# Kernel tuning notes

Hardware: AMD Instinct MI355X
Metric: run time of the kernel (lower is better)

The kernel has to match this reference:

```python
import jax, jax.numpy as jnp
import numpy as np

D = 1024
H = 16
DK = D // H

def setup_inputs() -> dict:
    key = jax.random.key(0)
    k1, k2, k3 = jax.random.split(key, 3)
    x = jax.random.normal(k1, (2, 2048, D), dtype=jnp.float32)
    # torch nn.Linear weight shapes: qkv [3D, D], o [D, D]; y = x @ W.T
    scale = 1.0 / np.sqrt(D)
    W_qkv = jax.random.normal(k2, (3 * D, D), dtype=jnp.float32) * scale
    W_o = jax.random.normal(k3, (D, D), dtype=jnp.float32) * scale
    return {"x": x, "W_qkv": W_qkv, "W_o": W_o}

def reference(x, W_qkv, W_o):
    B, T, _ = x.shape
    qkv = x @ W_qkv.T                                    # [B, T, 3D]
    qkv = qkv.reshape(B, T, 3, H, DK)
    qkv = jnp.transpose(qkv, (0, 3, 2, 1, 4))            # [B, H, 3, T, DK]
    q, k, v = qkv[:, :, 0], qkv[:, :, 1], qkv[:, :, 2]   # each [B, H, T, DK]
    scores = jnp.einsum("bhqd,bhkd->bhqk", q, k) / np.sqrt(DK)
    causal = jnp.tril(jnp.ones((T, T), dtype=bool))       # keep lower triangle
    scores = jnp.where(causal, scores, -jnp.inf)
    attn = jax.nn.softmax(scores, axis=-1)
    out = jnp.einsum("bhqk,bhkd->bhqd", attn, v)          # [B, H, T, DK]
    out = jnp.transpose(out, (0, 2, 1, 3)).reshape(B, T, H * DK)
    return out @ W_o.T
```

## Files before the change

### kernel.cpp

```cpp
#include <hip/hip_runtime.h>
#include <hip/hip_bf16.h>

typedef __bf16 bf16x8 __attribute__((ext_vector_type(8)));
typedef float f32x4 __attribute__((ext_vector_type(4)));
typedef unsigned int u32;
typedef u32 u32x4 __attribute__((ext_vector_type(4)));

#define MFMA(a, b, c) __builtin_amdgcn_mfma_f32_16x16x32_bf16((a), (b), (c), 0, 0, 0)

static __device__ __forceinline__ bf16x8 ld8(const __bf16* p) {
  return *reinterpret_cast<const bf16x8*>(p);
}

static __device__ __forceinline__ u32 pkbf(float a, float b) {
  union { __bf16 h; unsigned short s; } x, y;
  x.h = (__bf16)a; y.h = (__bf16)b;
  return (u32)x.s | ((u32)y.s << 16);
}

typedef unsigned int __attribute__((address_space(1))) gu32_t;
typedef unsigned int __attribute__((address_space(3))) lu32_t;
static __device__ __forceinline__ void gld16(const __bf16* g, __bf16* l) {
  __builtin_amdgcn_global_load_lds((const gu32_t*)(const void*)g,
                                   (lu32_t*)(void*)l, 16, 0, 0);
}

__global__ __launch_bounds__(256)
void cvt_f32_bf16(const float* __restrict__ a, __bf16* __restrict__ oa, int na,
                  const float* __restrict__ b, __bf16* __restrict__ ob) {
  const int i = blockIdx.x * 256 + threadIdx.x;
  const float* src; __bf16* dst; int e;
  if (i < (na >> 3)) { src = a; dst = oa; e = i << 3; }
  else { src = b; dst = ob; e = (i << 3) - na; }
  f32x4 v0 = *reinterpret_cast<const f32x4*>(src + e);
  f32x4 v1 = *reinterpret_cast<const f32x4*>(src + e + 4);
  bf16x8 o;
#pragma unroll
  for (int j = 0; j < 4; ++j) { o[j] = (__bf16)v0[j]; o[j + 4] = (__bf16)v1[j]; }
  *reinterpret_cast<bf16x8*>(dst + e) = o;
}

static __device__ __forceinline__ void stage8f(__bf16* __restrict__ dst,
                                               const float* __restrict__ src) {
  f32x4 a = *reinterpret_cast<const f32x4*>(src);
  f32x4 b = *reinterpret_cast<const f32x4*>(src + 4);
  bf16x8 o;
#pragma unroll
  for (int i = 0; i < 4; ++i) { o[i] = (__bf16)a[i]; o[i + 4] = (__bf16)b[i]; }
  *reinterpret_cast<bf16x8*>(dst) = o;
}

template<int BN, bool SPLIT, bool OUT_BF16, bool B_F32>
__global__ __launch_bounds__(256, 2)
void gemm3(const __bf16* __restrict__ A, const void* __restrict__ Wv,
           void* __restrict__ Cv, __bf16* __restrict__ VT,
           int M, int N, int K) {
  constexpr int NF = BN / 32;
  constexpr float SC2Q = 0.125f * 1.4426950408889634f;
  __shared__ __bf16 lA[128 * 64];
  __shared__ __bf16 lB[BN * 64];

  const int tid = threadIdx.x;
  const int ntiles = N / BN;
  const int mt = blockIdx.x / ntiles;
  const int nt = blockIdx.x % ntiles;
  const int m0 = mt << 7, n0 = nt * BN;
  const int lane = tid & 63, w = tid >> 6;
  const int wm = (w >> 1) << 6;
  const int wn = (w & 1) * (BN / 2);
  const int fr = lane & 15, fg = lane >> 4;

  f32x4 acc[4][NF] = {};

  for (int k0 = 0; k0 < K; k0 += 64) {
    __syncthreads();
#pragma unroll
    for (int jj = 0; jj < 4; ++jj) {
      const int q = (w << 2) | jj;
      const int v = (q << 6) | lane;
      const int row = v >> 3;
      const int cc = (v & 7) ^ (row & 7);
      gld16(A + (size_t)(m0 + row) * K + k0 + (cc << 3), lA + (q << 9));
    }
    if constexpr (B_F32) {
#pragma unroll
      for (int hh = 0; hh < BN / 64; ++hh) {
        const int row = (tid >> 2) + (hh << 6);
        const int c0 = (tid & 3) << 1;
        const float* src = (const float*)Wv + (size_t)(n0 + row) * K + k0 + (c0 << 3);
#pragma unroll
        for (int cg = 0; cg < 2; ++cg)
          stage8f(lB + (row << 6) + (((c0 + cg) ^ (row & 7)) << 3), src + (cg << 3));
      }
    } else {
#pragma unroll
      for (int jj = 0; jj < NF; ++jj) {
        const int q = w * NF + jj;
        const int v = (q << 6) | lane;
        const int row = v >> 3;
        const int cc = (v & 7) ^ (row & 7);
        gld16((const __bf16*)Wv + (size_t)(n0 + row) * K + k0 + (cc << 3), lB + (q << 9));
      }
    }
    __syncthreads();

    bf16x8 af[2][4], bfr[2][NF];
#pragma unroll
    for (int kc = 0; kc < 2; ++kc) {
#pragma unroll
      for (int m = 0; m < 4; ++m) {
        const int row = wm + m * 16 + fr;
        af[kc][m] = ld8(lA + (row << 6) + ((((kc << 2) | fg) ^ (row & 7)) << 3));
      }
#pragma unroll
      for (int n = 0; n < NF; ++n) {
        const int row = wn + n * 16 + fr;
        bfr[kc][n] = ld8(lB + (row << 6) + ((((kc << 2) | fg) ^ (row & 7)) << 3));
      }
    }
#pragma unroll
    for (int kc = 0; kc < 2; ++kc)
#pragma unroll
      for (int m = 0; m < 4; ++m)
#pragma unroll
        for (int n = 0; n < NF; ++n)
          acc[m][n] = MFMA(af[kc][m], bfr[kc][n], acc[m][n]);
  }

#pragma unroll
  for (int m = 0; m < 4; ++m) {
#pragma unroll
    for (int n = 0; n < NF; ++n) {
#pragma unroll
      for (int r = 0; r < 4; ++r) {
        int row = m0 + wm + m * 16 + fg * 4 + r;
        int col = n0 + wn + n * 16 + fr;
        float v = acc[m][n][r];
        if constexpr (SPLIT) {
          int b = row >> 11, t = row & 2047;
          if (col >= 2048) {
            VT[((size_t)(b << 10) + (col - 2048)) * 2048 + t] = (__bf16)v;
          } else {
            if (col < 1024) v *= SC2Q;
            ((__bf16*)Cv)[(size_t)row * 2048 + col] = (__bf16)v;
          }
        } else if constexpr (OUT_BF16) {
          ((__bf16*)Cv)[(size_t)row * N + col] = (__bf16)v;
        } else {
          ((float*)Cv)[(size_t)row * N + col] = v;
        }
      }
    }
  }
}

static __device__ __forceinline__ void softmax_step(
    f32x4 (&s)[4], f32x4 (&o)[4], float& m, float& l, bf16x8 (&pa)[2],
    bool diag, int q0wt, int k0, int fg, int fr) {
  constexpr float NEG = -1e30f;
  float sv[4][4];
#pragma unroll
  for (int n = 0; n < 4; ++n)
#pragma unroll
    for (int r = 0; r < 4; ++r) {
      float x = s[n][r];
      if (diag && (k0 + n * 16 + fg * 4 + r > q0wt + fr)) x = NEG;
      sv[n][r] = x;
    }

  float t0 = fmaxf(fmaxf(sv[0][0], sv[0][1]), fmaxf(sv[0][2], sv[0][3]));
  float t1 = fmaxf(fmaxf(sv[1][0], sv[1][1]), fmaxf(sv[1][2], sv[1][3]));
  float t2 = fmaxf(fmaxf(sv[2][0], sv[2][1]), fmaxf(sv[2][2], sv[2][3]));
  float t3 = fmaxf(fmaxf(sv[3][0], sv[3][1]), fmaxf(sv[3][2], sv[3][3]));
  float rm = fmaxf(fmaxf(t0, t1), fmaxf(t2, t3));
  rm = fmaxf(rm, __shfl_xor(rm, 16));
  rm = fmaxf(rm, __shfl_xor(rm, 32));

  if (!__all(rm <= m + 16.f)) {
    float mnew = fmaxf(m, rm);
    float alpha = __builtin_exp2f(m - mnew);
    m = mnew;
    l *= alpha;
    float ao[4];
#pragma unroll
    for (int r = 0; r < 4; ++r)
      ao[r] = __shfl(alpha, fg * 4 + r);
#pragma unroll
    for (int n = 0; n < 4; ++n)
#pragma unroll
      for (int r = 0; r < 4; ++r)
        o[n][r] *= ao[r];
  }

  float p[4][4];
#pragma unroll
  for (int n = 0; n < 4; ++n)
#pragma unroll
    for (int r = 0; r < 4; ++r)
      p[n][r] = __builtin_exp2f(sv[n][r] - m);

  float u0 = (p[0][0] + p[0][1]) + (p[0][2] + p[0][3]);
  float u1 = (p[1][0] + p[1][1]) + (p[1][2] + p[1][3]);
  float u2 = (p[2][0] + p[2][1]) + (p[2][2] + p[2][3]);
  float u3 = (p[3][0] + p[3][1]) + (p[3][2] + p[3][3]);
  float rs = (u0 + u1) + (u2 + u3);
  rs += __shfl_xor(rs, 16);
  rs += __shfl_xor(rs, 32);
  l += rs;

  u32 wpk[4][2];
#pragma unroll
  for (int n = 0; n < 4; ++n) {
    wpk[n][0] = pkbf(p[n][0], p[n][1]);
    wpk[n][1] = pkbf(p[n][2], p[n][3]);
  }

  u32 rcv[2][2][2];
#pragma unroll
  for (int e = 0; e < 2; ++e) {
    const int src = fr + ((((fg & 1) << 1) | ((fg >> 1) ^ e)) << 4);
    const bool tsel = ((fg & 1) ^ e) != 0;
#pragma unroll
    for (int c = 0; c < 2; ++c)
#pragma unroll
      for (int hh = 0; hh < 2; ++hh) {
        u32 v = tsel ? wpk[(c << 1) | 1][hh] : wpk[(c << 1) | 0][hh];
        rcv[e][c][hh] = (u32)__shfl((int)v, src);
      }
  }
  const bool hi = (fg >> 1) != 0;
  u32x4 w0, w1;
#pragma unroll
  for (int a = 0; a < 2; ++a)
#pragma unroll
    for (int hh = 0; hh < 2; ++hh) {
      w0[2 * a + hh] = hi ? rcv[a ^ 1][0][hh] : rcv[a][0][hh];
      w1[2 * a + hh] = hi ? rcv[a ^ 1][1][hh] : rcv[a][1][hh];
    }
  pa[0] = __builtin_bit_cast(bf16x8, w0);
  pa[1] = __builtin_bit_cast(bf16x8, w1);
}

static __device__ __forceinline__ void write_out(
    __bf16* __restrict__ out, f32x4 (&o)[4], float l,
    int b, int hoff, int q0wt, int fg, int fr) {
  float linv = 1.f / l;
  float lo[4];
#pragma unroll
  for (int r = 0; r < 4; ++r)
    lo[r] = __shfl(linv, fg * 4 + r);
#pragma unroll
  for (int n = 0; n < 4; ++n)
#pragma unroll
    for (int r = 0; r < 4; ++r) {
      int t = q0wt + fg * 4 + r;
      out[((size_t)(b * 2048 + t)) * 1024 + hoff + n * 16 + fr] = (__bf16)(o[n][r] * lo[r]);
    }
}

__global__ __launch_bounds__(256, 4)
void attn_causal10(const __bf16* __restrict__ qk, const __bf16* __restrict__ vt,
                   __bf16* __restrict__ out) {
  constexpr float NEG = -1e30f;

  __shared__ __bf16 lK[2][4096];
  __shared__ __bf16 lV[2][4096];

  const int tid = threadIdx.x;
  const int lane = tid & 63, w = tid >> 6;
  const int fr = lane & 15, fg = lane >> 4;
  const int blk = blockIdx.x;
  const int j = blk >> 3;
  const int bh = ((blk & 7) << 2) | (j & 3);
  const int qb = 31 - (j >> 2);
  const int b = bh >> 4, h = bh & 15;
  const int q0w = (qb << 6) + (w << 4);
  const int hoff = h * 64;
  const size_t qkbase = (size_t)b * (2048 * 2048);
  const __bf16* kb = qk + qkbase + 1024 + hoff;
  const __bf16* vtb = vt + (size_t)((b << 10) | hoff) * 2048;

  bf16x8 qf[2];
#pragma unroll
  for (int c = 0; c < 2; ++c)
    qf[c] = ld8(qk + qkbase + (size_t)(q0w + fr) * 2048 + hoff + c * 32 + fg * 8);

  f32x4 o[4] = {};
  float m = NEG;
  float l = 0.f;

#define STAGE(bf, k0s)                                                        \
  do {                                                                        \
    _Pragma("unroll")                                                         \
    for (int jj = 0; jj < 2; ++jj) {                                          \
      const int q = (w << 1) | jj;                                            \
      const int v = (q << 6) | lane;                                          \
      const int row = v >> 3;                                                 \
      const int cc = (v & 7) ^ (row & 7);                                     \
      gld16(kb + (size_t)((k0s) + row) * 2048 + (cc << 3), &lK[bf][q << 9]);  \
      gld16(vtb + (size_t)row * 2048 + (k0s) + (cc << 3), &lV[bf][q << 9]);   \
    }                                                                         \
  } while (0)

  int buf = 0;
  STAGE(0, 0);
  __syncthreads();

  for (int kt = 0; kt <= qb; ++kt) {
    const int k0 = kt << 6;
    if (kt < qb) STAGE(buf ^ 1, k0 + 64);

    f32x4 s[4] = {};
#pragma unroll
    for (int c = 0; c < 2; ++c) {
      bf16x8 kfc[4];
#pragma unroll
      for (int n = 0; n < 4; ++n) {
        const int row = n * 16 + fr;
        const int sc = ((c << 2) | fg) ^ (row & 7);
        kfc[n] = ld8(&lK[buf][(row << 6) + (sc << 3)]);
      }
#pragma unroll
      for (int n = 0; n < 4; ++n)
        s[n] = MFMA(kfc[n], qf[c], s[n]);
    }

    bf16x8 pa[2];
    softmax_step(s, o, m, l, pa, kt == qb, q0w, k0, fg, fr);

#pragma unroll
    for (int c = 0; c < 2; ++c) {
      bf16x8 vfc[4];
#pragma unroll
      for (int n = 0; n < 4; ++n) {
        const int row = n * 16 + fr;
        const int sc = ((c << 2) | fg) ^ (row & 7);
        vfc[n] = ld8(&lV[buf][(row << 6) + (sc << 3)]);
      }
#pragma unroll
      for (int n = 0; n < 4; ++n)
        o[n] = MFMA(pa[c], vfc[n], o[n]);
    }

    __syncthreads();
    buf ^= 1;
  }
#undef STAGE

  write_out(out, o, l, b, hoff, q0w, fg, fr);
}

extern "C" void kernel_launch(void* const* d_in, const int* in_sizes, int n_in,
                              void* d_out, int out_size, void* d_ws, size_t ws_size,
                              hipStream_t stream) {
  const float* x = (const float*)d_in[0];
  const float* w_qkv = (const float*)d_in[1];
  const float* w_o = (const float*)d_in[2];
  float* out = (float*)d_out;

  const int M = 4096;
  __bf16* qk = (__bf16*)d_ws;
  __bf16* vt = (__bf16*)((char*)d_ws + (size_t)M * 2048 * 2);
  __bf16* attn = (__bf16*)((char*)d_ws + (size_t)M * 3072 * 2);

  __bf16* xb = (__bf16*)d_out;
  __bf16* wqb = xb + 4194304;
  const int NX = 4194304;

  cvt_f32_bf16<<<3584, 256, 0, stream>>>(x, xb, NX, w_qkv, wqb);

  gemm3<128, true, true, false><<<(M / 128) * (3072 / 128), 256, 0, stream>>>(
      xb, (const void*)wqb, (void*)qk, vt, M, 3072, 1024);

  attn_causal10<<<1024, 256, 0, stream>>>(qk, vt, attn);

  gemm3<64, false, false, true><<<(M / 128) * (1024 / 64), 256, 0, stream>>>(
      attn, (const void*)w_o, (void*)out, nullptr, M, 1024, 1024);
}
```

Measured before the change: 121.5 us.

## Process two 16-row query tiles per wave in causal attention

The attention kernel now uses 2 waves per block instead of 4, and each wave handles two 16-row query sub-tiles (A and B) against the same K/V fragments loaded from LDS. This halves the LDS fragment reads per query row and doubles MFMA work per LDS load. Each thread now issues more staging loads. The cost is double the accumulator and softmax state registers per wave, fewer waves per block to hide latency, and a launch-bounds hint of 2 blocks per CU.

Result: slower. 142.5 us (+17.3%).

```diff
diff --git a/kernel.cpp b/kernel.cpp
--- a/kernel.cpp
+++ b/kernel.cpp
@@ -258,8 +258,8 @@
     }
 }
 
-__global__ __launch_bounds__(256, 4)
-void attn_causal10(const __bf16* __restrict__ qk, const __bf16* __restrict__ vt,
+__global__ __launch_bounds__(128, 2)
+void attn_causal11(const __bf16* __restrict__ qk, const __bf16* __restrict__ vt,
                    __bf16* __restrict__ out) {
   constexpr float NEG = -1e30f;
 
@@ -274,26 +274,28 @@
   const int bh = ((blk & 7) << 2) | (j & 3);
   const int qb = 31 - (j >> 2);
   const int b = bh >> 4, h = bh & 15;
-  const int q0w = (qb << 6) + (w << 4);
+  const int q0A = (qb << 6) + (w << 5);
+  const int q0B = q0A + 16;
   const int hoff = h * 64;
   const size_t qkbase = (size_t)b * (2048 * 2048);
   const __bf16* kb = qk + qkbase + 1024 + hoff;
   const __bf16* vtb = vt + (size_t)((b << 10) | hoff) * 2048;
 
-  bf16x8 qf[2];
-#pragma unroll
-  for (int c = 0; c < 2; ++c)
-    qf[c] = ld8(qk + qkbase + (size_t)(q0w + fr) * 2048 + hoff + c * 32 + fg * 8);
-
-  f32x4 o[4] = {};
-  float m = NEG;
-  float l = 0.f;
+  bf16x8 qfA[2], qfB[2];
+#pragma unroll
+  for (int c = 0; c < 2; ++c) {
+    qfA[c] = ld8(qk + qkbase + (size_t)(q0A + fr) * 2048 + hoff + c * 32 + fg * 8);
+    qfB[c] = ld8(qk + qkbase + (size_t)(q0B + fr) * 2048 + hoff + c * 32 + fg * 8);
+  }
+
+  f32x4 oA[4] = {}, oB[4] = {};
+  float mA = NEG, lA_ = 0.f, mB = NEG, lB_ = 0.f;
 
 #define STAGE(bf, k0s)                                                        \
   do {                                                                        \
     _Pragma("unroll")                                                         \
-    for (int jj = 0; jj < 2; ++jj) {                                          \
-      const int q = (w << 1) | jj;                                            \
+    for (int jj = 0; jj < 4; ++jj) {                                          \
+      const int q = (w << 2) | jj;                                            \
       const int v = (q << 6) | lane;                                          \
       const int row = v >> 3;                                                 \
       const int cc = (v & 7) ^ (row & 7);                                     \
@@ -310,7 +312,7 @@
     const int k0 = kt << 6;
     if (kt < qb) STAGE(buf ^ 1, k0 + 64);
 
-    f32x4 s[4] = {};
+    f32x4 sA[4] = {}, sB[4] = {};
 #pragma unroll
     for (int c = 0; c < 2; ++c) {
       bf16x8 kfc[4];
@@ -322,11 +324,16 @@
       }
 #pragma unroll
       for (int n = 0; n < 4; ++n)
-        s[n] = MFMA(kfc[n], qf[c], s[n]);
-    }
-
-    bf16x8 pa[2];
-    softmax_step(s, o, m, l, pa, kt == qb, q0w, k0, fg, fr);
+        sA[n] = MFMA(kfc[n], qfA[c], sA[n]);
+#pragma unroll
+      for (int n = 0; n < 4; ++n)
+        sB[n] = MFMA(kfc[n], qfB[c], sB[n]);
+    }
+
+    const bool diag = (kt == qb);
+    bf16x8 paA[2], paB[2];
+    softmax_step(sA, oA, mA, lA_, paA, diag, q0A, k0, fg, fr);
+    softmax_step(sB, oB, mB, lB_, paB, diag, q0B, k0, fg, fr);
 
 #pragma unroll
     for (int c = 0; c < 2; ++c) {
@@ -339,7 +346,10 @@
       }
 #pragma unroll
       for (int n = 0; n < 4; ++n)
-        o[n] = MFMA(pa[c], vfc[n], o[n]);
+        oA[n] = MFMA(paA[c], vfc[n], oA[n]);
+#pragma unroll
+      for (int n = 0; n < 4; ++n)
+        oB[n] = MFMA(paB[c], vfc[n], oB[n]);
     }
 
     __syncthreads();
@@ -347,7 +357,8 @@
   }
 #undef STAGE
 
-  write_out(out, o, l, b, hoff, q0w, fg, fr);
+  write_out(out, oA, lA_, b, hoff, q0A, fg, fr);
+  write_out(out, oB, lB_, b, hoff, q0B, fg, fr);
 }
 
 extern "C" void kernel_launch(void* const* d_in, const int* in_sizes, int n_in,
@@ -372,7 +383,7 @@
   gemm3<128, true, true, false><<<(M / 128) * (3072 / 128), 256, 0, stream>>>(
       xb, (const void*)wqb, (void*)qk, vt, M, 3072, 1024);
 
-  attn_causal10<<<1024, 256, 0, stream>>>(qk, vt, attn);
+  attn_causal11<<<1024, 128, 0, stream>>>(qk, vt, attn);
 
   gemm3<64, false, false, true><<<(M / 128) * (1024 / 64), 256, 0, stream>>>(
       attn, (const void*)w_o, (void*)out, nullptr, M, 1024, 1024);
```
